# Kernel optimization log

Measured on AMD Instinct MI355X. Metric: run time of the kernel, lower is better.

Reference implementation:

```python
import jax, jax.numpy as jnp
import numpy as np

D_MODEL = 1024
D_FF = 4096
N = 16384


def setup_inputs() -> dict:
    key = jax.random.key(0)
    k_b, k_w1, k_b1, k_w2, k_b2 = jax.random.split(key, 5)
    s1 = 1.0 / np.sqrt(D_MODEL)
    s2 = 1.0 / np.sqrt(D_FF)
    return {
        "batch": jax.random.normal(k_b, (N, D_MODEL), dtype=jnp.float32),
        # nn.Linear stores weight as [out_features, in_features]
        "W1": jax.random.uniform(k_w1, (D_FF, D_MODEL), jnp.float32, -s1, s1),
        "b1": jax.random.uniform(k_b1, (D_FF,), jnp.float32, -s1, s1),
        "W2": jax.random.uniform(k_w2, (D_MODEL, D_FF), jnp.float32, -s2, s2),
        "b2": jax.random.uniform(k_b2, (D_MODEL,), jnp.float32, -s2, s2),
    }


def reference(batch, W1, b1, W2, b2):
    # inner = tanh(linear1(batch)) : [N, d_ff]
    inner = jnp.tanh(batch @ W1.T + b1)
    # wx = tanh(linear2(inner)) : [N, d_model]
    wx = jnp.tanh(inner @ W2.T + b2)
    # diag(wx @ batch.T) == row-wise dot product, avoids O(N^2) matmul
    return jax.nn.sigmoid(jnp.sum(wx * batch, axis=-1))  # [N]
```

## Files before the change

### kernel.cpp

```cpp
#include <hip/hip_runtime.h>
#include <math.h>

#define N_ROWS 16384
#define DMODEL 1024
#define DFF    4096

typedef _Float16 f16;
typedef __attribute__((ext_vector_type(4))) _Float16 f16x4;
typedef __attribute__((ext_vector_type(8))) _Float16 f16x8;
typedef __attribute__((ext_vector_type(4))) float f32x4;

__device__ inline void async_ld16(const f16* g, f16* l) {
  __builtin_amdgcn_global_load_lds(
      (__attribute__((address_space(1))) void*)(g),
      (__attribute__((address_space(3))) void*)(l),
      16, 0, 0);
}

__global__ void cast_to_f16(const float* __restrict__ src, f16* __restrict__ dst, int n) {
  int i = (blockIdx.x * blockDim.x + threadIdx.x) * 8;
  if (i >= n) return;
  float4 v0 = ((const float4*)(src + i))[0];
  float4 v1 = ((const float4*)(src + i))[1];
  f16x8 h = { (f16)v0.x, (f16)v0.y, (f16)v0.z, (f16)v0.w,
              (f16)v1.x, (f16)v1.y, (f16)v1.z, (f16)v1.w };
  *(f16x8*)(dst + i) = h;
}

template <int K, typename OUT_T>
__global__ __launch_bounds__(256, 3)
void gemm_bt_tanh(const f16* __restrict__ A, const f16* __restrict__ B,
                  const float* __restrict__ bias, OUT_T* __restrict__ C, int Nc) {
  __shared__ __align__(16) f16 As[128 * 32];
  __shared__ __align__(16) f16 Bs[128 * 32];

  const int tid  = threadIdx.x;
  const int lane = tid & 63;
  const int wave = tid >> 6;
  const size_t row0 = (size_t)blockIdx.x * 128;
  const size_t col0 = (size_t)blockIdx.y * 128;
  const int wm = (wave >> 1) * 64;
  const int wn = (wave & 1) * 64;
  const int fr = lane & 15;
  const int fk = (lane >> 4) * 8;

  const int srow   = tid >> 2;
  const int schunk = (tid & 3) * 8;
  const f16* Ap = A + (row0 + srow) * (size_t)K + schunk;
  const f16* Bp = B + (col0 + srow) * (size_t)K + schunk;
  f16* Asd = As + tid * 8;
  f16* Bsd = Bs + tid * 8;

  f32x4 acc[4][4] = {};

  for (int k0 = 0; k0 < K; k0 += 32) {
    __syncthreads();
    async_ld16(Ap + k0, Asd);
    async_ld16(Ap + (size_t)64 * K + k0, Asd + 2048);
    async_ld16(Bp + k0, Bsd);
    async_ld16(Bp + (size_t)64 * K + k0, Bsd + 2048);
    __syncthreads();

    f16x8 af[4], bf[4];
#pragma unroll
    for (int i = 0; i < 4; ++i) {
      af[i] = *(const f16x8*)(As + (wm + i * 16 + fr) * 32 + fk);
      bf[i] = *(const f16x8*)(Bs + (wn + i * 16 + fr) * 32 + fk);
    }
#pragma unroll
    for (int i = 0; i < 4; ++i)
#pragma unroll
      for (int j = 0; j < 4; ++j)
        acc[i][j] = __builtin_amdgcn_mfma_f32_16x16x32_f16(af[i], bf[j], acc[i][j], 0, 0, 0);
  }

  const int erow = wm + (lane >> 4) * 4;
  const int ecol = wn + fr;
#pragma unroll
  for (int i = 0; i < 4; ++i) {
#pragma unroll
    for (int j = 0; j < 4; ++j) {
      size_t gcol = col0 + ecol + j * 16;
      float b = bias[gcol];
#pragma unroll
      for (int r = 0; r < 4; ++r) {
        size_t grow = row0 + erow + i * 16 + r;
        C[grow * (size_t)Nc + gcol] = (OUT_T)tanhf(acc[i][j][r] + b);
      }
    }
  }
}

__global__ void rowdot_sigmoid(const f16* __restrict__ wx, const float* __restrict__ batch,
                               float* __restrict__ out) {
  const int row = blockIdx.x;
  const int t = threadIdx.x;
  const f16* wr = wx + (size_t)row * DMODEL + t * 4;
  const float* br = batch + (size_t)row * DMODEL + t * 4;
  f16x4 h = *(const f16x4*)wr;
  float4 b4 = *(const float4*)br;
  float s = (float)h[0] * b4.x + (float)h[1] * b4.y + (float)h[2] * b4.z + (float)h[3] * b4.w;
#pragma unroll
  for (int off = 32; off > 0; off >>= 1) s += __shfl_down(s, off, 64);
  __shared__ float partial[4];
  if ((t & 63) == 0) partial[t >> 6] = s;
  __syncthreads();
  if (t == 0) {
    float tot = partial[0] + partial[1] + partial[2] + partial[3];
    out[row] = 1.0f / (1.0f + expf(-tot));
  }
}

extern "C" void kernel_launch(void* const* d_in, const int* in_sizes, int n_in,
                              void* d_out, int out_size, void* d_ws, size_t ws_size,
                              hipStream_t stream) {
  const float* batch = (const float*)d_in[0];
  const float* W1    = (const float*)d_in[1];
  const float* b1    = (const float*)d_in[2];
  const float* W2    = (const float*)d_in[3];
  const float* b2    = (const float*)d_in[4];
  float* out = (float*)d_out;

  char* ws = (char*)d_ws;
  f16* batch_h = (f16*)ws;  ws += (size_t)N_ROWS * DMODEL * sizeof(f16);
  f16* W1_h    = (f16*)ws;  ws += (size_t)DFF * DMODEL * sizeof(f16);
  f16* W2_h    = (f16*)ws;  ws += (size_t)DMODEL * DFF * sizeof(f16);
  f16* inner_h = (f16*)ws;  ws += (size_t)N_ROWS * DFF * sizeof(f16);
  f16* wx_h    = (f16*)ws;  ws += (size_t)N_ROWS * DMODEL * sizeof(f16);

  const int nb  = N_ROWS * DMODEL;
  const int nw  = DFF * DMODEL;
  cast_to_f16<<<nb / 2048, 256, 0, stream>>>(batch, batch_h, nb);
  cast_to_f16<<<nw / 2048, 256, 0, stream>>>(W1, W1_h, nw);
  cast_to_f16<<<nw / 2048, 256, 0, stream>>>(W2, W2_h, nw);

  dim3 g1(N_ROWS / 128, DFF / 128);
  gemm_bt_tanh<DMODEL, f16><<<g1, 256, 0, stream>>>(batch_h, W1_h, b1, inner_h, DFF);
  dim3 g2(N_ROWS / 128, DMODEL / 128);
  gemm_bt_tanh<DFF, f16><<<g2, 256, 0, stream>>>(inner_h, W2_h, b2, wx_h, DMODEL);

  rowdot_sigmoid<<<N_ROWS, 256, 0, stream>>>(wx_h, batch, out);
}
```

Baseline: 487.9 us.

## Merge cast kernels, use fast exp-based tanh, raise GEMM occupancy bound

Fuses the three fp32-to-fp16 cast launches into one kernel that indexes across all three buffers. It also replaces tanhf in the GEMM epilogues with an __expf-based formula, uses __expf in the sigmoid, and raises the launch-bounds occupancy hint from 3 to 4 blocks. These target launch overhead, epilogue transcendental cost and latency hiding. The fast tanh loses some accuracy and can produce NaN for large inputs (inf/inf is avoided here, but overflow gives 1-0 = 1, which is fine). The tighter register budget may cause spills.

```diff
diff --git a/kernel.cpp b/kernel.cpp
--- a/kernel.cpp
+++ b/kernel.cpp
@@ -17,20 +17,31 @@
       16, 0, 0);
 }
 
-__global__ void cast_to_f16(const float* __restrict__ src, f16* __restrict__ dst, int n) {
-  int i = (blockIdx.x * blockDim.x + threadIdx.x) * 8;
-  if (i >= n) return;
-  float4 v0 = ((const float4*)(src + i))[0];
-  float4 v1 = ((const float4*)(src + i))[1];
+__device__ inline float fast_tanh(float x) {
+  float t = __expf(2.0f * x);
+  return 1.0f - 2.0f / (t + 1.0f);
+}
+
+__global__ void cast3_to_f16(const float* __restrict__ a, f16* __restrict__ ah, int na,
+                             const float* __restrict__ b, f16* __restrict__ bh, int nb,
+                             const float* __restrict__ c, f16* __restrict__ ch, int nc) {
+  long i = (long)(blockIdx.x * blockDim.x + threadIdx.x) * 8;
+  const float* s; f16* d;
+  if (i < na)                { s = a + i;            d = ah + i; }
+  else if (i < na + nb)      { s = b + (i - na);     d = bh + (i - na); }
+  else if (i < na + nb + nc) { s = c + (i - na - nb); d = ch + (i - na - nb); }
+  else return;
+  float4 v0 = ((const float4*)s)[0];
+  float4 v1 = ((const float4*)s)[1];
   f16x8 h = { (f16)v0.x, (f16)v0.y, (f16)v0.z, (f16)v0.w,
               (f16)v1.x, (f16)v1.y, (f16)v1.z, (f16)v1.w };
-  *(f16x8*)(dst + i) = h;
+  *(f16x8*)d = h;
 }
 
-template <int K, typename OUT_T>
-__global__ __launch_bounds__(256, 3)
+template <int K>
+__global__ __launch_bounds__(256, 4)
 void gemm_bt_tanh(const f16* __restrict__ A, const f16* __restrict__ B,
-                  const float* __restrict__ bias, OUT_T* __restrict__ C, int Nc) {
+                  const float* __restrict__ bias, f16* __restrict__ C, int Nc) {
   __shared__ __align__(16) f16 As[128 * 32];
   __shared__ __align__(16) f16 Bs[128 * 32];
 
@@ -85,7 +96,7 @@
 #pragma unroll
       for (int r = 0; r < 4; ++r) {
         size_t grow = row0 + erow + i * 16 + r;
-        C[grow * (size_t)Nc + gcol] = (OUT_T)tanhf(acc[i][j][r] + b);
+        C[grow * (size_t)Nc + gcol] = (f16)fast_tanh(acc[i][j][r] + b);
       }
     }
   }
@@ -107,7 +118,7 @@
   __syncthreads();
   if (t == 0) {
     float tot = partial[0] + partial[1] + partial[2] + partial[3];
-    out[row] = 1.0f / (1.0f + expf(-tot));
+    out[row] = 1.0f / (1.0f + __expf(-tot));
   }
 }
 
@@ -128,16 +139,16 @@
   f16* inner_h = (f16*)ws;  ws += (size_t)N_ROWS * DFF * sizeof(f16);
   f16* wx_h    = (f16*)ws;  ws += (size_t)N_ROWS * DMODEL * sizeof(f16);
 
-  const int nb  = N_ROWS * DMODEL;
-  const int nw  = DFF * DMODEL;
-  cast_to_f16<<<nb / 2048, 256, 0, stream>>>(batch, batch_h, nb);
-  cast_to_f16<<<nw / 2048, 256, 0, stream>>>(W1, W1_h, nw);
-  cast_to_f16<<<nw / 2048, 256, 0, stream>>>(W2, W2_h, nw);
+  const int nb = N_ROWS * DMODEL;
+  const int nw = DFF * DMODEL;
+  const int total8 = (nb + nw + nw) / 8;
+  cast3_to_f16<<<total8 / 256, 256, 0, stream>>>(batch, batch_h, nb,
+                                                 W1, W1_h, nw, W2, W2_h, nw);
 
   dim3 g1(N_ROWS / 128, DFF / 128);
-  gemm_bt_tanh<DMODEL, f16><<<g1, 256, 0, stream>>>(batch_h, W1_h, b1, inner_h, DFF);
+  gemm_bt_tanh<DMODEL><<<g1, 256, 0, stream>>>(batch_h, W1_h, b1, inner_h, DFF);
   dim3 g2(N_ROWS / 128, DMODEL / 128);
-  gemm_bt_tanh<DFF, f16><<<g2, 256, 0, stream>>>(inner_h, W2_h, b2, wx_h, DMODEL);
+  gemm_bt_tanh<DFF><<<g2, 256, 0, stream>>>(inner_h, W2_h, b2, wx_h, DMODEL);
 
   rowdot_sigmoid<<<N_ROWS, 256, 0, stream>>>(wx_h, batch, out);
 }
```

Result: faster. 471.1 us (-3.4%).
